# Kernel optimization log

Hardware: AMD Instinct MI355X
Metric: run time of the kernel (lower is better)

The kernel has to match this reference:

```python
import jax, jax.numpy as jnp
import numpy as np
from jax import lax

TOP_K = 6
NORM_MIN = 1e-12


def setup_inputs() -> dict:
    key = jax.random.key(0)
    k0, k1, k2, k3, k4, k5 = jax.random.split(key, 6)
    B, S, H, E, I = 2, 1024, 2048, 64, 512
    return {
        "hidden_states": jax.random.normal(k0, (B, S, H), dtype=jnp.float32),
        "gate_w": jax.random.normal(k1, (E, H), dtype=jnp.float32) * 0.02,
        "e_bias": jax.random.normal(k2, (E,), dtype=jnp.float32) * 0.01,
        "gate_proj": jax.random.normal(k3, (E, H, I), dtype=jnp.float32) * 0.02,
        "up_proj": jax.random.normal(k4, (E, H, I), dtype=jnp.float32) * 0.02,
        "down_proj": jax.random.normal(k5, (E, I, H), dtype=jnp.float32) * 0.02,
    }


def reference(hidden_states, gate_w, e_bias, gate_proj, up_proj, down_proj):
    B, S, H = hidden_states.shape
    E = gate_w.shape[0]
    x = hidden_states.reshape(-1, H)                      # [T, H]
    T = x.shape[0]

    # --- routing (done in float32 in the original) ---
    router_logits = x.astype(jnp.float32) @ gate_w.T      # [T, E]
    routing_probs = jax.nn.softmax(router_logits, axis=-1)
    # topk over bias-corrected scores, but weights come from raw probs
    _, selected = lax.top_k(routing_probs + e_bias[None, :], TOP_K)  # [T, k]
    w = jnp.take_along_axis(routing_probs, selected, axis=-1)        # [T, k]
    w = w / jnp.clip(w.sum(axis=-1, keepdims=True), NORM_MIN)
    w = w.astype(hidden_states.dtype)

    # combine weights: [T, E], zero for unselected experts
    combine = jnp.zeros((T, E), dtype=hidden_states.dtype)
    combine = combine.at[jnp.arange(T)[:, None], selected].add(w)

    # --- experts: SwiGLU MLP per expert, weighted-sum combine ---
    def step(acc, params):
        wg, wu, wd, c = params                            # wg,wu [H,I]; wd [I,H]; c [T]
        h = jax.nn.silu(x @ wg) * (x @ wu)                # [T, I]
        return acc + (h @ wd) * c[:, None], None

    init = jnp.zeros((T, H), dtype=hidden_states.dtype)
    final, _ = lax.scan(step, init, (gate_proj, up_proj, down_proj, combine.T))
    return final.reshape(-1), router_logits.reshape(-1)
```

## Files before the change

### kernel.cpp

```cpp
#include <hip/hip_runtime.h>
#include <math.h>

#define T_TOK 2048
#define H_DIM 2048
#define E_NUM 64
#define I_DIM 512
#define TOPK  6
#define NPAIR (T_TOK * TOPK)
#define MAXTILES 80

typedef __attribute__((ext_vector_type(8))) short s8;
typedef __attribute__((ext_vector_type(4))) float f4;
typedef __attribute__((ext_vector_type(8))) unsigned short u16x8;

static __device__ __forceinline__ unsigned short f2bf(float f) {
  unsigned int u = __float_as_uint(f);
  u += 0x7fff + ((u >> 16) & 1);
  return (unsigned short)(u >> 16);
}
static __device__ __forceinline__ unsigned int cvt_pk(float lo, float hi) {
  unsigned int r;
  asm("v_cvt_pk_bf16_f32 %0, %1, %2" : "=v"(r) : "v"(lo), "v"(hi));
  return r;
}
static __device__ __forceinline__ void gload_lds16(const void* g, void* l) {
  __builtin_amdgcn_global_load_lds(
      (const __attribute__((address_space(1))) unsigned int*)g,
      (__attribute__((address_space(3))) unsigned int*)l, 16, 0, 0);
}
#define SBAR()      __builtin_amdgcn_s_barrier()
#define SCHED0()    __builtin_amdgcn_sched_barrier(0)
#define WAIT_LGKM0() asm volatile("s_waitcnt lgkmcnt(0)" ::: "memory")
#define WAIT_VM0()   asm volatile("s_waitcnt vmcnt(0)" ::: "memory")
#define WAIT_VM2()   asm volatile("s_waitcnt vmcnt(2)" ::: "memory")
#define WAIT_VM4()   asm volatile("s_waitcnt vmcnt(4)" ::: "memory")
#define WAIT_VM6()   asm volatile("s_waitcnt vmcnt(6)" ::: "memory")

__global__ __launch_bounds__(512) void router_kernel(
    const float* __restrict__ x, const float* __restrict__ gw,
    const float* __restrict__ ebias, float* __restrict__ logits_out,
    int* __restrict__ sel, float* __restrict__ wsel)
{
  __shared__ float xs[4][H_DIM];
  __shared__ float lg[4][E_NUM];
  int t0 = blockIdx.x * 4;
  int tid = threadIdx.x;
  {
    float4* xsv = (float4*)&xs[0][0];
    const float4* src = (const float4*)(x + (size_t)t0 * H_DIM);
    for (int i = tid; i < 4 * H_DIM / 4; i += 512) xsv[i] = src[i];
  }
  __syncthreads();

  int wave = tid >> 6, lane = tid & 63;
  for (int ii = 0; ii < 4; ++ii) {
    int e0 = wave * 8 + ii * 2, e1 = e0 + 1;
    const float4* g0 = (const float4*)(gw + (size_t)e0 * H_DIM);
    const float4* g1 = (const float4*)(gw + (size_t)e1 * H_DIM);
    float s00=0.f,s01=0.f,s02=0.f,s03=0.f, s10=0.f,s11=0.f,s12=0.f,s13=0.f;
    for (int h4 = lane; h4 < H_DIM / 4; h4 += 64) {
      float4 w0 = g0[h4], w1 = g1[h4];
      float4 a0 = ((const float4*)xs[0])[h4];
      float4 a1 = ((const float4*)xs[1])[h4];
      float4 a2 = ((const float4*)xs[2])[h4];
      float4 a3 = ((const float4*)xs[3])[h4];
      s00 += w0.x*a0.x + w0.y*a0.y + w0.z*a0.z + w0.w*a0.w;
      s01 += w0.x*a1.x + w0.y*a1.y + w0.z*a1.z + w0.w*a1.w;
      s02 += w0.x*a2.x + w0.y*a2.y + w0.z*a2.z + w0.w*a2.w;
      s03 += w0.x*a3.x + w0.y*a3.y + w0.z*a3.z + w0.w*a3.w;
      s10 += w1.x*a0.x + w1.y*a0.y + w1.z*a0.z + w1.w*a0.w;
      s11 += w1.x*a1.x + w1.y*a1.y + w1.z*a1.z + w1.w*a1.w;
      s12 += w1.x*a2.x + w1.y*a2.y + w1.z*a2.z + w1.w*a2.w;
      s13 += w1.x*a3.x + w1.y*a3.y + w1.z*a3.z + w1.w*a3.w;
    }
    for (int off = 32; off; off >>= 1) {
      s00 += __shfl_down(s00, off); s01 += __shfl_down(s01, off);
      s02 += __shfl_down(s02, off); s03 += __shfl_down(s03, off);
      s10 += __shfl_down(s10, off); s11 += __shfl_down(s11, off);
      s12 += __shfl_down(s12, off); s13 += __shfl_down(s13, off);
    }
    if (lane == 0) {
      lg[0][e0]=s00; lg[1][e0]=s01; lg[2][e0]=s02; lg[3][e0]=s03;
      lg[0][e1]=s10; lg[1][e1]=s11; lg[2][e1]=s12; lg[3][e1]=s13;
    }
  }
  __syncthreads();

  if (tid < 256) {
    int tt = tid >> 6, e = tid & 63;
    logits_out[(size_t)(t0 + tt) * E_NUM + e] = lg[tt][e];
  }

  if (wave == 0) {
    for (int tt = 0; tt < 4; ++tt) {
      int t = t0 + tt;
      float v = lg[tt][lane];
      float m = v;
      for (int off = 32; off; off >>= 1) m = fmaxf(m, __shfl_xor(m, off));
      float ex = __expf(v - m);
      float sum = ex;
      for (int off = 32; off; off >>= 1) sum += __shfl_xor(sum, off);
      float prob = ex / sum;
      float sc = prob + ebias[lane];

      int selidx[TOPK]; float selw[TOPK]; float wsum = 0.f;
      #pragma unroll
      for (int k = 0; k < TOPK; ++k) {
        float mm = sc;
        for (int off = 32; off; off >>= 1) mm = fmaxf(mm, __shfl_xor(mm, off));
        unsigned long long ball = __ballot(sc == mm);
        int s = __ffsll(ball) - 1;
        float p = __shfl(prob, s);
        selidx[k] = s; selw[k] = p; wsum += p;
        if (lane == s) sc = -INFINITY;
      }
      if (lane == 0) {
        float inv = 1.f / fmaxf(wsum, 1e-12f);
        #pragma unroll
        for (int k = 0; k < TOPK; ++k) {
          sel[t * TOPK + k] = selidx[k];
          wsel[t * TOPK + k] = selw[k] * inv;
        }
      }
    }
  }
}

__global__ __launch_bounds__(64) void build_lists(
    const int* __restrict__ sel, const float* __restrict__ wsel,
    int* __restrict__ cnt, int* __restrict__ toklist, float* __restrict__ wtlist,
    int* __restrict__ posmap)
{
  int e = blockIdx.x, lane = threadIdx.x;
  int base = 0;
  for (int t0 = 0; t0 < T_TOK; t0 += 64) {
    int t = t0 + lane;
    int flag = 0, kk = 0; float w = 0.f;
    #pragma unroll
    for (int k = 0; k < TOPK; ++k)
      if (sel[t * TOPK + k] == e) { flag = 1; kk = k; w = wsel[t * TOPK + k]; }
    unsigned long long b = __ballot(flag);
    int pos = base + __popcll(b & ((1ull << lane) - 1ull));
    if (flag) {
      toklist[e * T_TOK + pos] = t;
      wtlist[e * T_TOK + pos] = w;
      posmap[t * TOPK + kk] = pos;
    }
    base += __popcll(b);
  }
  if (lane == 0) cnt[e] = base;
}

__global__ void scan_kernel(const int* __restrict__ cnt, int* __restrict__ texp,
                            int* __restrict__ tmap, int* __restrict__ ntile) {
  if (threadIdx.x == 0) {
    int nt = 0;
    for (int e = 0; e < E_NUM; ++e) {
      texp[e] = nt;
      int m = (cnt[e] + 255) >> 8;
      for (int tb = 0; tb < m && nt < MAXTILES; ++tb) tmap[nt++] = e * 16 + tb;
    }
    *ntile = nt;
  }
}

__global__ __launch_bounds__(256) void permute_kernel(
    const float* __restrict__ x, const int* __restrict__ cnt,
    const int* __restrict__ toklist, const int* __restrict__ tmap,
    const int* __restrict__ ntile, unsigned short* __restrict__ xt)
{
  int tile = blockIdx.y;
  if (tile >= *ntile) return;
  int ks = blockIdx.x;
  int em = tmap[tile], e = em >> 4, tb = em & 15;
  int n = cnt[e];
  int r = threadIdx.x;
  int tok = toklist[e * T_TOK + min(tb * 256 + r, n - 1)];
  const float4* src = (const float4*)(x + (size_t)tok * H_DIM + ks * 32);
  float4 v[8];
  #pragma unroll
  for (int q = 0; q < 8; ++q) v[q] = src[q];
  int g = (r >> 1) & 3;
  unsigned short* dst = xt + ((size_t)(tile * 64 + ks) * 1024 + r * 4) * 8;
  #pragma unroll
  for (int u = 0; u < 4; ++u) {
    int k16 = u ^ g;
    float4 a = v[2 * k16], b = v[2 * k16 + 1];
    u16x8 p;
    ((unsigned int*)&p)[0] = cvt_pk(a.x, a.y);
    ((unsigned int*)&p)[1] = cvt_pk(a.z, a.w);
    ((unsigned int*)&p)[2] = cvt_pk(b.x, b.y);
    ((unsigned int*)&p)[3] = cvt_pk(b.z, b.w);
    *(u16x8*)(dst + u * 8) = p;
  }
}

__global__ __launch_bounds__(512, 4) void gateup_kernel(
    const unsigned short* __restrict__ xt, const float* __restrict__ gp,
    const float* __restrict__ up, const int* __restrict__ tmap,
    const int* __restrict__ ntile, unsigned short* __restrict__ hat)
{
  __shared__ __align__(16) unsigned short A_lds[2][8192];
  __shared__ __align__(16) unsigned int   Bt[2][2][64 * 20];
  int tile = blockIdx.x;
  if (tile >= *ntile) return;
  int e = tmap[tile] >> 4;
  int ic = blockIdx.y, colbase = ic * 64;
  int tid = threadIdx.x, lane = tid & 63, wave = tid >> 6;
  int matc = wave >> 2, cw = wave & 3;
  int lrow = (lane >> 4) * 4, lcol = lane & 15, kgl = lane >> 4;
  int hp = tid & 15, cb = (tid >> 4) & 15, mstage = tid >> 8;
  const float* bsrc0 = ((mstage == 0) ? gp : up)
      + (size_t)e * (H_DIM * I_DIM) + colbase + (size_t)(2 * hp) * I_DIM + cb * 4;
  const unsigned short* achunk0 = xt + (size_t)tile * 64 * 1024 * 8;

  f4 acc[4][4];
  #pragma unroll
  for (int a = 0; a < 4; ++a)
    #pragma unroll
    for (int b = 0; b < 4; ++b) acc[a][b] = (f4)0.f;

  float4 p0, p1, q0, q1;
  {
    const unsigned short* s = achunk0 + (size_t)(wave * 128 + lane) * 8;
    gload_lds16(s,       &A_lds[0][(wave * 128) * 8]);
    gload_lds16(s + 512, &A_lds[0][(wave * 128 + 64) * 8]);
    p0 = *(const float4*)bsrc0;
    p1 = *(const float4*)(bsrc0 + I_DIM);
    WAIT_VM0();
    unsigned int* db = &Bt[0][mstage][cb * 4 * 20 + hp];
    db[0]  = cvt_pk(p0.x, p1.x); db[20] = cvt_pk(p0.y, p1.y);
    db[40] = cvt_pk(p0.z, p1.z); db[60] = cvt_pk(p0.w, p1.w);
    const float* b1 = bsrc0 + (size_t)32 * I_DIM;
    q0 = *(const float4*)b1;
    q1 = *(const float4*)(b1 + I_DIM);
    WAIT_LGKM0();
    SBAR();
    SCHED0();
  }

#define GU_STEP(K, C0, C1, N0, N1) do {                                            \
    if ((K) + 1 < 64) {                                                            \
      const unsigned short* s = achunk0 + ((size_t)((K) + 1) * 1024 + wave * 128 + lane) * 8; \
      gload_lds16(s,       &A_lds[((K) + 1) & 1][(wave * 128) * 8]);               \
      gload_lds16(s + 512, &A_lds[((K) + 1) & 1][(wave * 128 + 64) * 8]);          \
    }                                                                              \
    if ((K) + 2 < 64) {                                                            \
      const float* b = bsrc0 + (size_t)((K) + 2) * 32 * I_DIM;                     \
      N0 = *(const float4*)b; N1 = *(const float4*)(b + I_DIM);                    \
    }                                                                              \
    if ((K) + 2 < 64)      { WAIT_VM4(); }                                         \
    else if ((K) + 1 < 64) { WAIT_VM2(); }                                         \
    else                   { WAIT_VM0(); }                                         \
    if ((K) + 1 < 64) {                                                            \
      unsigned int* db = &Bt[((K) + 1) & 1][mstage][cb * 4 * 20 + hp];             \
      db[0]  = cvt_pk(C0.x, C1.x); db[20] = cvt_pk(C0.y, C1.y);                    \
      db[40] = cvt_pk(C0.z, C1.z); db[60] = cvt_pk(C0.w, C1.w);                    \
    }                                                                              \
    {                                                                              \
      s8 afr[4];                                                                   \
      _Pragma("unroll")                                                            \
      for (int mf = 0; mf < 4; ++mf) {                                             \
        int r = cw * 64 + mf * 16 + lcol;                                          \
        afr[mf] = *(s8*)&A_lds[(K) & 1][r * 32 + ((kgl ^ ((r >> 1) & 3)) * 8)];    \
      }                                                                            \
      _Pragma("unroll")                                                            \
      for (int nf = 0; nf < 4; ++nf) {                                             \
        s8 bfr = *(s8*)&Bt[(K) & 1][matc][(nf * 16 + lcol) * 20 + kgl * 4];        \
        _Pragma("unroll")                                                          \
        for (int mf = 0; mf < 4; ++mf)                                             \
          acc[mf][nf] = __builtin_amdgcn_mfma_f32_16x16x32_bf16(afr[mf], bfr, acc[mf][nf], 0, 0, 0); \
      }                                                                            \
    }                                                                              \
    if ((K) + 1 < 64) {                                                            \
      if ((K) + 2 < 64) { WAIT_VM2(); } else { WAIT_VM0(); }                       \
      WAIT_LGKM0(); SBAR(); SCHED0();                                              \
    }                                                                              \
  } while (0)

  for (int k = 0; k < 64; k += 2) {
    GU_STEP(k,     q0, q1, p0, p1);
    GU_STEP(k + 1, p0, p1, q0, q1);
  }
#undef GU_STEP

  f4* exch = (f4*)&Bt[0][0][0];
  unsigned short* hs = &A_lds[0][0];
  #pragma unroll
  for (int nf = 0; nf < 4; ++nf) {
    __syncthreads();
    if (wave >= 4) {
      #pragma unroll
      for (int mf = 0; mf < 4; ++mf)
        exch[((wave - 4) * 4 + mf) * 64 + lane] = acc[mf][nf];
    }
    __syncthreads();
    if (wave < 4) {
      #pragma unroll
      for (int mf = 0; mf < 4; ++mf) {
        f4 u = exch[(wave * 4 + mf) * 64 + lane];
        #pragma unroll
        for (int j = 0; j < 4; ++j) {
          float g = acc[mf][nf][j];
          float h = g / (1.f + __expf(-g)) * u[j];
          hs[(wave * 64 + mf * 16 + lrow + j) * 64 + nf * 16 + lcol] = f2bf(h);
        }
      }
    }
  }
  __syncthreads();
  #pragma unroll
  for (int c = 0; c < 2; ++c) {
    unsigned short* base = hat + (size_t)(tile * 16 + ic * 2 + c) * 1024 * 8;
    for (int uu = tid; uu < 1024; uu += 512) {
      int row = uu >> 2, k16 = (uu & 3) ^ ((row >> 1) & 3);
      *(u16x8*)(base + (size_t)uu * 8) = *(const u16x8*)&hs[row * 64 + c * 32 + k16 * 8];
    }
  }
}

__global__ __launch_bounds__(256, 4) void down_kernel(
    const unsigned short* __restrict__ hat, const float* __restrict__ dp,
    const int* __restrict__ cnt, const int* __restrict__ tmap,
    const int* __restrict__ ntile, const float* __restrict__ wtlist,
    unsigned short* __restrict__ pout)
{
  __shared__ __align__(16) unsigned short A_lds[2][8192];
  __shared__ __align__(16) unsigned int   Bt[2][64 * 20];
  __shared__ float swt[256];
  int tile = blockIdx.x;
  if (tile >= *ntile) return;
  int em = tmap[tile], e = em >> 4, tb = em & 15;
  int n = cnt[e];
  int hc = blockIdx.y, colbase = hc * 64;
  int tid = threadIdx.x, lane = tid & 63, wave = tid >> 6, wbase = wave * 64;
  int lrow = (lane >> 4) * 4, lcol = lane & 15, kgl = lane >> 4;
  int hp = tid & 15, cb = tid >> 4;
  const float* bsrc0 = dp + (size_t)e * (I_DIM * H_DIM) + colbase
                       + (size_t)(2 * hp) * H_DIM + cb * 4;
  const unsigned short* achunk0 = hat + (size_t)tile * 16 * 1024 * 8;

  int rr = tb * 256 + tid;
  swt[tid] = (rr < n) ? wtlist[e * T_TOK + rr] : 0.f;

  f4 acc[4][4];
  #pragma unroll
  for (int a = 0; a < 4; ++a)
    #pragma unroll
    for (int b = 0; b < 4; ++b) acc[a][b] = (f4)0.f;

  float4 p0, p1, q0, q1;
  {
    const unsigned short* s = achunk0 + (size_t)(wave * 256 + lane) * 8;
    #pragma unroll
    for (int i = 0; i < 4; ++i)
      gload_lds16(s + i * 512, &A_lds[0][(wave * 256 + i * 64) * 8]);
    p0 = *(const float4*)bsrc0;
    p1 = *(const float4*)(bsrc0 + H_DIM);
    WAIT_VM0();
    unsigned int* db = &Bt[0][cb * 4 * 20 + hp];
    db[0]  = cvt_pk(p0.x, p1.x); db[20] = cvt_pk(p0.y, p1.y);
    db[40] = cvt_pk(p0.z, p1.z); db[60] = cvt_pk(p0.w, p1.w);
    const float* b1 = bsrc0 + (size_t)32 * H_DIM;
    q0 = *(const float4*)b1;
    q1 = *(const float4*)(b1 + H_DIM);
    WAIT_LGKM0();
    SBAR();
    SCHED0();
  }

#define DN_STEP(K, C0, C1, N0, N1) do {                                            \
    if ((K) + 1 < 16) {                                                            \
      const unsigned short* s = achunk0 + ((size_t)((K) + 1) * 1024 + wave * 256 + lane) * 8; \
      _Pragma("unroll")                                                            \
      for (int i = 0; i < 4; ++i)                                                  \
        gload_lds16(s + i * 512, &A_lds[((K) + 1) & 1][(wave * 256 + i * 64) * 8]);\
    }                                                                              \
    if ((K) + 2 < 16) {                                                            \
      const float* b = bsrc0 + (size_t)((K) + 2) * 32 * H_DIM;                     \
      N0 = *(const float4*)b; N1 = *(const float4*)(b + H_DIM);                    \
    }                                                                              \
    if ((K) + 2 < 16)      { WAIT_VM6(); }                                         \
    else if ((K) + 1 < 16) { WAIT_VM4(); }                                         \
    else                   { WAIT_VM0(); }                                         \
    if ((K) + 1 < 16) {                                                            \
      unsigned int* db = &Bt[((K) + 1) & 1][cb * 4 * 20 + hp];                     \
      db[0]  = cvt_pk(C0.x, C1.x); db[20] = cvt_pk(C0.y, C1.y);                    \
      db[40] = cvt_pk(C0.z, C1.z); db[60] = cvt_pk(C0.w, C1.w);                    \
    }                                                                              \
    {                                                                              \
      s8 afr[4];                                                                   \
      _Pragma("unroll")                                                            \
      for (int mf = 0; mf < 4; ++mf) {                                             \
        int r = wbase + mf * 16 + lcol;                                            \
        afr[mf] = *(s8*)&A_lds[(K) & 1][r * 32 + ((kgl ^ ((r >> 1) & 3)) * 8)];    \
      }                                                                            \
      _Pragma("unroll")                                                            \
      for (int nf = 0; nf < 4; ++nf) {                                             \
        s8 bfr = *(s8*)&Bt[(K) & 1][(nf * 16 + lcol) * 20 + kgl * 4];              \
        _Pragma("unroll")                                                          \
        for (int mf = 0; mf < 4; ++mf)                                             \
          acc[mf][nf] = __builtin_amdgcn_mfma_f32_16x16x32_bf16(afr[mf], bfr, acc[mf][nf], 0, 0, 0); \
      }                                                                            \
    }                                                                              \
    if ((K) + 1 < 16) {                                                            \
      if ((K) + 2 < 16) { WAIT_VM2(); } else { WAIT_VM0(); }                       \
      WAIT_LGKM0(); SBAR(); SCHED0();                                              \
    }                                                                              \
  } while (0)

  for (int k = 0; k < 16; k += 2) {
    DN_STEP(k,     q0, q1, p0, p1);
    DN_STEP(k + 1, p0, p1, q0, q1);
  }
#undef DN_STEP

  __syncthreads();
  unsigned short* hs = &A_lds[0][0];
  #pragma unroll
  for (int mf = 0; mf < 4; ++mf)
    #pragma unroll
    for (int nf = 0; nf < 4; ++nf)
      #pragma unroll
      for (int j = 0; j < 4; ++j) {
        int r = wbase + mf * 16 + lrow + j;
        hs[r * 64 + nf * 16 + lcol] = f2bf(acc[mf][nf][j] * swt[r]);
      }
  __syncthreads();
  for (int u = tid; u < 2048; u += 256) {
    int row = u >> 3, unit = u & 7;
    *(u16x8*)(pout + (size_t)(tile * 256 + row) * H_DIM + colbase + unit * 8) =
        *(const u16x8*)&hs[row * 64 + unit * 8];
  }
}

__global__ __launch_bounds__(256) void reduce_kernel(
    const unsigned short* __restrict__ pout, const int* __restrict__ sel,
    const int* __restrict__ posmap, const int* __restrict__ texp,
    float* __restrict__ out)
{
  int t = blockIdx.x, tid = threadIdx.x;
  int col = tid * 8;
  float acc[8];
  #pragma unroll
  for (int j = 0; j < 8; ++j) acc[j] = 0.f;
  #pragma unroll
  for (int k = 0; k < TOPK; ++k) {
    int e = sel[t * TOPK + k];
    int row = texp[e] * 256 + posmap[t * TOPK + k];
    u16x8 v = *(const u16x8*)(pout + (size_t)row * H_DIM + col);
    #pragma unroll
    for (int j = 0; j < 8; ++j)
      acc[j] += __uint_as_float((unsigned int)(unsigned short)v[j] << 16);
  }
  float4 o0 = {acc[0], acc[1], acc[2], acc[3]};
  float4 o1 = {acc[4], acc[5], acc[6], acc[7]};
  *(float4*)(out + (size_t)t * H_DIM + col)     = o0;
  *(float4*)(out + (size_t)t * H_DIM + col + 4) = o1;
}

extern "C" void kernel_launch(void* const* d_in, const int* in_sizes, int n_in,
                              void* d_out, int out_size, void* d_ws, size_t ws_size,
                              hipStream_t stream) {
  const float* hidden = (const float*)d_in[0];
  const float* gate_w = (const float*)d_in[1];
  const float* e_bias = (const float*)d_in[2];
  const float* gate_p = (const float*)d_in[3];
  const float* up_p   = (const float*)d_in[4];
  const float* down_p = (const float*)d_in[5];

  float* out_final  = (float*)d_out;
  float* out_logits = out_final + (size_t)T_TOK * H_DIM;

  int*   cnt     = (int*)d_ws;
  int*   texp    = cnt + 64;
  int*   ntile   = texp + 64;
  int*   tmap    = ntile + 16;
  int*   sel     = tmap + MAXTILES;
  float* wsel    = (float*)(sel + NPAIR);
  int*   posmap  = (int*)(wsel + NPAIR);
  int*   toklist = posmap + NPAIR;
  float* wtlist  = (float*)(toklist + E_NUM * T_TOK);
  unsigned short* xt  = (unsigned short*)(wtlist + E_NUM * T_TOK);
  unsigned short* hat = xt + (size_t)MAXTILES * 64 * 1024 * 8;
  unsigned short* pout = xt;

  router_kernel<<<T_TOK / 4, 512, 0, stream>>>(hidden, gate_w, e_bias, out_logits, sel, wsel);
  build_lists<<<E_NUM, 64, 0, stream>>>(sel, wsel, cnt, toklist, wtlist, posmap);
  scan_kernel<<<1, 64, 0, stream>>>(cnt, texp, tmap, ntile);
  permute_kernel<<<dim3(64, MAXTILES), 256, 0, stream>>>(hidden, cnt, toklist, tmap, ntile, xt);
  gateup_kernel<<<dim3(MAXTILES, I_DIM / 64), 512, 0, stream>>>(
      xt, gate_p, up_p, tmap, ntile, hat);
  down_kernel<<<dim3(MAXTILES, H_DIM / 64), 256, 0, stream>>>(
      hat, down_p, cnt, tmap, ntile, wtlist, pout);
  reduce_kernel<<<T_TOK, 256, 0, stream>>>(pout, sel, posmap, texp, out_final);
}
```

Before: 536.2 us.

## Widen down_kernel tile to 128 columns with 512 threads sharing A tile

The down-projection kernel now uses 512 threads per block covering 128 output columns, split into two column groups of four waves that share one staged A (activation) tile in LDS. Each A chunk is loaded once per block instead of once per 64 columns, which halves the A-traffic and the number of blocks. The epilogue writes the two column halves in two passes through the reused LDS buffer, adding barriers. Launch bounds of 512 threads with 4 blocks per SM may raise register pressure and lower occupancy.

```diff
diff --git a/kernel.cpp b/kernel.cpp
--- a/kernel.cpp
+++ b/kernel.cpp
@@ -34,7 +34,6 @@
 #define WAIT_VM0()   asm volatile("s_waitcnt vmcnt(0)" ::: "memory")
 #define WAIT_VM2()   asm volatile("s_waitcnt vmcnt(2)" ::: "memory")
 #define WAIT_VM4()   asm volatile("s_waitcnt vmcnt(4)" ::: "memory")
-#define WAIT_VM6()   asm volatile("s_waitcnt vmcnt(6)" ::: "memory")
 
 __global__ __launch_bounds__(512) void router_kernel(
     const float* __restrict__ x, const float* __restrict__ gw,
@@ -319,29 +318,32 @@
   }
 }
 
-__global__ __launch_bounds__(256, 4) void down_kernel(
+__global__ __launch_bounds__(512, 4) void down_kernel(
     const unsigned short* __restrict__ hat, const float* __restrict__ dp,
     const int* __restrict__ cnt, const int* __restrict__ tmap,
     const int* __restrict__ ntile, const float* __restrict__ wtlist,
     unsigned short* __restrict__ pout)
 {
   __shared__ __align__(16) unsigned short A_lds[2][8192];
-  __shared__ __align__(16) unsigned int   Bt[2][64 * 20];
+  __shared__ __align__(16) unsigned int   Bt[2][2][64 * 20];
   __shared__ float swt[256];
   int tile = blockIdx.x;
   if (tile >= *ntile) return;
   int em = tmap[tile], e = em >> 4, tb = em & 15;
   int n = cnt[e];
-  int hc = blockIdx.y, colbase = hc * 64;
-  int tid = threadIdx.x, lane = tid & 63, wave = tid >> 6, wbase = wave * 64;
+  int hc = blockIdx.y, colbase = hc * 128;
+  int tid = threadIdx.x, lane = tid & 63, wave = tid >> 6;
+  int rg = wave & 3, cg = wave >> 2;
   int lrow = (lane >> 4) * 4, lcol = lane & 15, kgl = lane >> 4;
-  int hp = tid & 15, cb = tid >> 4;
-  const float* bsrc0 = dp + (size_t)e * (I_DIM * H_DIM) + colbase
+  int hp = tid & 15, cb = (tid >> 4) & 15, cgs = tid >> 8;
+  const float* bsrc0 = dp + (size_t)e * (I_DIM * H_DIM) + colbase + cgs * 64
                        + (size_t)(2 * hp) * H_DIM + cb * 4;
   const unsigned short* achunk0 = hat + (size_t)tile * 16 * 1024 * 8;
 
-  int rr = tb * 256 + tid;
-  swt[tid] = (rr < n) ? wtlist[e * T_TOK + rr] : 0.f;
+  if (tid < 256) {
+    int rr = tb * 256 + tid;
+    swt[tid] = (rr < n) ? wtlist[e * T_TOK + rr] : 0.f;
+  }
 
   f4 acc[4][4];
   #pragma unroll
@@ -351,14 +353,13 @@
 
   float4 p0, p1, q0, q1;
   {
-    const unsigned short* s = achunk0 + (size_t)(wave * 256 + lane) * 8;
-    #pragma unroll
-    for (int i = 0; i < 4; ++i)
-      gload_lds16(s + i * 512, &A_lds[0][(wave * 256 + i * 64) * 8]);
+    const unsigned short* s = achunk0 + (size_t)(wave * 128 + lane) * 8;
+    gload_lds16(s,       &A_lds[0][(wave * 128) * 8]);
+    gload_lds16(s + 512, &A_lds[0][(wave * 128 + 64) * 8]);
     p0 = *(const float4*)bsrc0;
     p1 = *(const float4*)(bsrc0 + H_DIM);
     WAIT_VM0();
-    unsigned int* db = &Bt[0][cb * 4 * 20 + hp];
+    unsigned int* db = &Bt[0][cgs][cb * 4 * 20 + hp];
     db[0]  = cvt_pk(p0.x, p1.x); db[20] = cvt_pk(p0.y, p1.y);
     db[40] = cvt_pk(p0.z, p1.z); db[60] = cvt_pk(p0.w, p1.w);
     const float* b1 = bsrc0 + (size_t)32 * H_DIM;
@@ -371,20 +372,19 @@
 
 #define DN_STEP(K, C0, C1, N0, N1) do {                                            \
     if ((K) + 1 < 16) {                                                            \
-      const unsigned short* s = achunk0 + ((size_t)((K) + 1) * 1024 + wave * 256 + lane) * 8; \
-      _Pragma("unroll")                                                            \
-      for (int i = 0; i < 4; ++i)                                                  \
-        gload_lds16(s + i * 512, &A_lds[((K) + 1) & 1][(wave * 256 + i * 64) * 8]);\
+      const unsigned short* s = achunk0 + ((size_t)((K) + 1) * 1024 + wave * 128 + lane) * 8; \
+      gload_lds16(s,       &A_lds[((K) + 1) & 1][(wave * 128) * 8]);               \
+      gload_lds16(s + 512, &A_lds[((K) + 1) & 1][(wave * 128 + 64) * 8]);          \
     }                                                                              \
     if ((K) + 2 < 16) {                                                            \
       const float* b = bsrc0 + (size_t)((K) + 2) * 32 * H_DIM;                     \
       N0 = *(const float4*)b; N1 = *(const float4*)(b + H_DIM);                    \
     }                                                                              \
-    if ((K) + 2 < 16)      { WAIT_VM6(); }                                         \
-    else if ((K) + 1 < 16) { WAIT_VM4(); }                                         \
+    if ((K) + 2 < 16)      { WAIT_VM4(); }                                         \
+    else if ((K) + 1 < 16) { WAIT_VM2(); }                                         \
     else                   { WAIT_VM0(); }                                         \
     if ((K) + 1 < 16) {                                                            \
-      unsigned int* db = &Bt[((K) + 1) & 1][cb * 4 * 20 + hp];                     \
+      unsigned int* db = &Bt[((K) + 1) & 1][cgs][cb * 4 * 20 + hp];                \
       db[0]  = cvt_pk(C0.x, C1.x); db[20] = cvt_pk(C0.y, C1.y);                    \
       db[40] = cvt_pk(C0.z, C1.z); db[60] = cvt_pk(C0.w, C1.w);                    \
     }                                                                              \
@@ -392,12 +392,12 @@
       s8 afr[4];                                                                   \
       _Pragma("unroll")                                                            \
       for (int mf = 0; mf < 4; ++mf) {                                             \
-        int r = wbase + mf * 16 + lcol;                                            \
+        int r = rg * 64 + mf * 16 + lcol;                                          \
         afr[mf] = *(s8*)&A_lds[(K) & 1][r * 32 + ((kgl ^ ((r >> 1) & 3)) * 8)];    \
       }                                                                            \
       _Pragma("unroll")                                                            \
       for (int nf = 0; nf < 4; ++nf) {                                             \
-        s8 bfr = *(s8*)&Bt[(K) & 1][(nf * 16 + lcol) * 20 + kgl * 4];              \
+        s8 bfr = *(s8*)&Bt[(K) & 1][cg][(nf * 16 + lcol) * 20 + kgl * 4];          \
         _Pragma("unroll")                                                          \
         for (int mf = 0; mf < 4; ++mf)                                             \
           acc[mf][nf] = __builtin_amdgcn_mfma_f32_16x16x32_bf16(afr[mf], bfr, acc[mf][nf], 0, 0, 0); \
@@ -418,19 +418,25 @@
   __syncthreads();
   unsigned short* hs = &A_lds[0][0];
   #pragma unroll
-  for (int mf = 0; mf < 4; ++mf)
-    #pragma unroll
-    for (int nf = 0; nf < 4; ++nf)
+  for (int pass = 0; pass < 2; ++pass) {
+    if (cg == pass) {
       #pragma unroll
-      for (int j = 0; j < 4; ++j) {
-        int r = wbase + mf * 16 + lrow + j;
-        hs[r * 64 + nf * 16 + lcol] = f2bf(acc[mf][nf][j] * swt[r]);
-      }
-  __syncthreads();
-  for (int u = tid; u < 2048; u += 256) {
-    int row = u >> 3, unit = u & 7;
-    *(u16x8*)(pout + (size_t)(tile * 256 + row) * H_DIM + colbase + unit * 8) =
-        *(const u16x8*)&hs[row * 64 + unit * 8];
+      for (int mf = 0; mf < 4; ++mf)
+        #pragma unroll
+        for (int nf = 0; nf < 4; ++nf)
+          #pragma unroll
+          for (int j = 0; j < 4; ++j) {
+            int r = rg * 64 + mf * 16 + lrow + j;
+            hs[r * 64 + nf * 16 + lcol] = f2bf(acc[mf][nf][j] * swt[r]);
+          }
+    }
+    __syncthreads();
+    for (int u = tid; u < 2048; u += 512) {
+      int row = u >> 3, unit = u & 7;
+      *(u16x8*)(pout + (size_t)(tile * 256 + row) * H_DIM + colbase + pass * 64 + unit * 8) =
+          *(const u16x8*)&hs[row * 64 + unit * 8];
+    }
+    __syncthreads();
   }
 }
 
@@ -491,7 +497,7 @@
   permute_kernel<<<dim3(64, MAXTILES), 256, 0, stream>>>(hidden, cnt, toklist, tmap, ntile, xt);
   gateup_kernel<<<dim3(MAXTILES, I_DIM / 64), 512, 0, stream>>>(
       xt, gate_p, up_p, tmap, ntile, hat);
-  down_kernel<<<dim3(MAXTILES, H_DIM / 64), 256, 0, stream>>>(
+  down_kernel<<<dim3(MAXTILES, H_DIM / 128), 512, 0, stream>>>(
       hat, down_p, cnt, tmap, ntile, wtlist, pout);
   reduce_kernel<<<T_TOK, 256, 0, stream>>>(pout, sel, posmap, texp, out_final);
 }
```

After: 520.3 us. 1.03x faster.

## Split gate/up GEMM into separate blocks and add standalone SwiGLU kernel

Applied to the files above, without the earlier changes.

The fused 512-thread gate+up kernel, where each block computed both matrices and exchanged accumulators through LDS, becomes a 256-thread kernel that computes one matrix per block, with the matrix chosen by a new grid z dimension. Gate and up outputs go to a bf16 scratch buffer, and a new swiglu kernel combines them into the swizzled layout the down kernel expects. This doubles the number of blocks and removes the multi-barrier exchange epilogue, which could improve occupancy and scheduling. In exchange it adds a kernel launch and an extra global round trip for the intermediates. The intermediates are also rounded to bf16 before the SiLU, which changes numerics slightly. The down kernel also swaps its cb/hp thread index mapping.

```diff
diff --git a/kernel.cpp b/kernel.cpp
--- a/kernel.cpp
+++ b/kernel.cpp
@@ -17,6 +17,9 @@
   unsigned int u = __float_as_uint(f);
   u += 0x7fff + ((u >> 16) & 1);
   return (unsigned short)(u >> 16);
+}
+static __device__ __forceinline__ float bf2f(unsigned short v) {
+  return __uint_as_float((unsigned int)v << 16);
 }
 static __device__ __forceinline__ unsigned int cvt_pk(float lo, float hi) {
   unsigned int r;
@@ -195,22 +198,22 @@
   }
 }
 
-__global__ __launch_bounds__(512, 4) void gateup_kernel(
+__global__ __launch_bounds__(256, 4) void gu_kernel(
     const unsigned short* __restrict__ xt, const float* __restrict__ gp,
     const float* __restrict__ up, const int* __restrict__ tmap,
-    const int* __restrict__ ntile, unsigned short* __restrict__ hat)
+    const int* __restrict__ ntile, unsigned short* __restrict__ gub)
 {
   __shared__ __align__(16) unsigned short A_lds[2][8192];
-  __shared__ __align__(16) unsigned int   Bt[2][2][64 * 20];
+  __shared__ __align__(16) unsigned int   Bt[2][64 * 20];
   int tile = blockIdx.x;
   if (tile >= *ntile) return;
   int e = tmap[tile] >> 4;
-  int ic = blockIdx.y, colbase = ic * 64;
+  int ic = blockIdx.y, mat = blockIdx.z, colbase = ic * 64;
   int tid = threadIdx.x, lane = tid & 63, wave = tid >> 6;
-  int matc = wave >> 2, cw = wave & 3;
+  int cw = wave;
   int lrow = (lane >> 4) * 4, lcol = lane & 15, kgl = lane >> 4;
-  int hp = tid & 15, cb = (tid >> 4) & 15, mstage = tid >> 8;
-  const float* bsrc0 = ((mstage == 0) ? gp : up)
+  int cb = tid & 15, hp = tid >> 4;
+  const float* bsrc0 = (mat ? up : gp)
       + (size_t)e * (H_DIM * I_DIM) + colbase + (size_t)(2 * hp) * I_DIM + cb * 4;
   const unsigned short* achunk0 = xt + (size_t)tile * 64 * 1024 * 8;
 
@@ -222,13 +225,14 @@
 
   float4 p0, p1, q0, q1;
   {
-    const unsigned short* s = achunk0 + (size_t)(wave * 128 + lane) * 8;
-    gload_lds16(s,       &A_lds[0][(wave * 128) * 8]);
-    gload_lds16(s + 512, &A_lds[0][(wave * 128 + 64) * 8]);
+    const unsigned short* s = achunk0 + (size_t)(wave * 256 + lane) * 8;
+    #pragma unroll
+    for (int i = 0; i < 4; ++i)
+      gload_lds16(s + i * 512, &A_lds[0][(wave * 256 + i * 64) * 8]);
     p0 = *(const float4*)bsrc0;
     p1 = *(const float4*)(bsrc0 + I_DIM);
     WAIT_VM0();
-    unsigned int* db = &Bt[0][mstage][cb * 4 * 20 + hp];
+    unsigned int* db = &Bt[0][cb * 4 * 20 + hp];
     db[0]  = cvt_pk(p0.x, p1.x); db[20] = cvt_pk(p0.y, p1.y);
     db[40] = cvt_pk(p0.z, p1.z); db[60] = cvt_pk(p0.w, p1.w);
     const float* b1 = bsrc0 + (size_t)32 * I_DIM;
@@ -241,19 +245,20 @@
 
 #define GU_STEP(K, C0, C1, N0, N1) do {                                            \
     if ((K) + 1 < 64) {                                                            \
-      const unsigned short* s = achunk0 + ((size_t)((K) + 1) * 1024 + wave * 128 + lane) * 8; \
-      gload_lds16(s,       &A_lds[((K) + 1) & 1][(wave * 128) * 8]);               \
-      gload_lds16(s + 512, &A_lds[((K) + 1) & 1][(wave * 128 + 64) * 8]);          \
+      const unsigned short* s = achunk0 + ((size_t)((K) + 1) * 1024 + wave * 256 + lane) * 8; \
+      _Pragma("unroll")                                                            \
+      for (int i = 0; i < 4; ++i)                                                  \
+        gload_lds16(s + i * 512, &A_lds[((K) + 1) & 1][(wave * 256 + i * 64) * 8]);\
     }                                                                              \
     if ((K) + 2 < 64) {                                                            \
       const float* b = bsrc0 + (size_t)((K) + 2) * 32 * I_DIM;                     \
       N0 = *(const float4*)b; N1 = *(const float4*)(b + I_DIM);                    \
     }                                                                              \
-    if ((K) + 2 < 64)      { WAIT_VM4(); }                                         \
-    else if ((K) + 1 < 64) { WAIT_VM2(); }                                         \
+    if ((K) + 2 < 64)      { WAIT_VM6(); }                                         \
+    else if ((K) + 1 < 64) { WAIT_VM4(); }                                         \
     else                   { WAIT_VM0(); }                                         \
     if ((K) + 1 < 64) {                                                            \
-      unsigned int* db = &Bt[((K) + 1) & 1][mstage][cb * 4 * 20 + hp];             \
+      unsigned int* db = &Bt[((K) + 1) & 1][cb * 4 * 20 + hp];                     \
       db[0]  = cvt_pk(C0.x, C1.x); db[20] = cvt_pk(C0.y, C1.y);                    \
       db[40] = cvt_pk(C0.z, C1.z); db[60] = cvt_pk(C0.w, C1.w);                    \
     }                                                                              \
@@ -266,7 +271,7 @@
       }                                                                            \
       _Pragma("unroll")                                                            \
       for (int nf = 0; nf < 4; ++nf) {                                             \
-        s8 bfr = *(s8*)&Bt[(K) & 1][matc][(nf * 16 + lcol) * 20 + kgl * 4];        \
+        s8 bfr = *(s8*)&Bt[(K) & 1][(nf * 16 + lcol) * 20 + kgl * 4];              \
         _Pragma("unroll")                                                          \
         for (int mf = 0; mf < 4; ++mf)                                             \
           acc[mf][nf] = __builtin_amdgcn_mfma_f32_16x16x32_bf16(afr[mf], bfr, acc[mf][nf], 0, 0, 0); \
@@ -284,38 +289,49 @@
   }
 #undef GU_STEP
 
-  f4* exch = (f4*)&Bt[0][0][0];
+  __syncthreads();
   unsigned short* hs = &A_lds[0][0];
   #pragma unroll
-  for (int nf = 0; nf < 4; ++nf) {
-    __syncthreads();
-    if (wave >= 4) {
+  for (int mf = 0; mf < 4; ++mf)
+    #pragma unroll
+    for (int nf = 0; nf < 4; ++nf)
       #pragma unroll
-      for (int mf = 0; mf < 4; ++mf)
-        exch[((wave - 4) * 4 + mf) * 64 + lane] = acc[mf][nf];
-    }
-    __syncthreads();
-    if (wave < 4) {
-      #pragma unroll
-      for (int mf = 0; mf < 4; ++mf) {
-        f4 u = exch[(wave * 4 + mf) * 64 + lane];
-        #pragma unroll
-        for (int j = 0; j < 4; ++j) {
-          float g = acc[mf][nf][j];
-          float h = g / (1.f + __expf(-g)) * u[j];
-          hs[(wave * 64 + mf * 16 + lrow + j) * 64 + nf * 16 + lcol] = f2bf(h);
-        }
+      for (int j = 0; j < 4; ++j) {
+        int r = cw * 64 + mf * 16 + lrow + j;
+        hs[r * 64 + nf * 16 + lcol] = f2bf(acc[mf][nf][j]);
       }
-    }
-  }
   __syncthreads();
-  #pragma unroll
-  for (int c = 0; c < 2; ++c) {
-    unsigned short* base = hat + (size_t)(tile * 16 + ic * 2 + c) * 1024 * 8;
-    for (int uu = tid; uu < 1024; uu += 512) {
-      int row = uu >> 2, k16 = (uu & 3) ^ ((row >> 1) & 3);
-      *(u16x8*)(base + (size_t)uu * 8) = *(const u16x8*)&hs[row * 64 + c * 32 + k16 * 8];
-    }
+  unsigned short* base = gub + ((size_t)((mat * MAXTILES + tile) * 8 + ic)) * 16384;
+  for (int u = tid; u < 2048; u += 256) {
+    int row = u >> 3, unit = u & 7;
+    *(u16x8*)(base + (size_t)row * 64 + unit * 8) = *(const u16x8*)&hs[row * 64 + unit * 8];
+  }
+}
+
+__global__ __launch_bounds__(256) void swiglu_kernel(
+    const unsigned short* __restrict__ gub, const int* __restrict__ ntile,
+    unsigned short* __restrict__ hat)
+{
+  int tile = blockIdx.y;
+  if (tile >= *ntile) return;
+  int c = blockIdx.x;
+  int ic = c >> 1, half = c & 1;
+  const unsigned short* gsrc = gub + ((size_t)(tile * 8 + ic)) * 16384;
+  const unsigned short* usrc = gsrc + (size_t)MAXTILES * 8 * 16384;
+  unsigned short* dst = hat + (size_t)(tile * 16 + c) * 1024 * 8;
+  for (int uu = threadIdx.x; uu < 1024; uu += 256) {
+    int row = uu >> 2, k16 = (uu & 3) ^ ((row >> 1) & 3);
+    size_t off = (size_t)row * 64 + half * 32 + k16 * 8;
+    u16x8 gv = *(const u16x8*)(gsrc + off);
+    u16x8 uv = *(const u16x8*)(usrc + off);
+    u16x8 hv;
+    #pragma unroll
+    for (int j = 0; j < 8; ++j) {
+      float gf = bf2f((unsigned short)gv[j]);
+      float uf = bf2f((unsigned short)uv[j]);
+      hv[j] = f2bf(gf / (1.f + __expf(-gf)) * uf);
+    }
+    *(u16x8*)(dst + (size_t)uu * 8) = hv;
   }
 }
 
@@ -333,9 +349,10 @@
   int em = tmap[tile], e = em >> 4, tb = em & 15;
   int n = cnt[e];
   int hc = blockIdx.y, colbase = hc * 64;
-  int tid = threadIdx.x, lane = tid & 63, wave = tid >> 6, wbase = wave * 64;
+  int tid = threadIdx.x, lane = tid & 63, wave = tid >> 6;
+  int wbase = wave * 64;
   int lrow = (lane >> 4) * 4, lcol = lane & 15, kgl = lane >> 4;
-  int hp = tid & 15, cb = tid >> 4;
+  int cb = tid & 15, hp = tid >> 4;
   const float* bsrc0 = dp + (size_t)e * (I_DIM * H_DIM) + colbase
                        + (size_t)(2 * hp) * H_DIM + cb * 4;
   const unsigned short* achunk0 = hat + (size_t)tile * 16 * 1024 * 8;
@@ -483,14 +500,16 @@
   float* wtlist  = (float*)(toklist + E_NUM * T_TOK);
   unsigned short* xt  = (unsigned short*)(wtlist + E_NUM * T_TOK);
   unsigned short* hat = xt + (size_t)MAXTILES * 64 * 1024 * 8;
+  unsigned short* gub = hat + (size_t)MAXTILES * 16 * 1024 * 8;
   unsigned short* pout = xt;
 
   router_kernel<<<T_TOK / 4, 512, 0, stream>>>(hidden, gate_w, e_bias, out_logits, sel, wsel);
   build_lists<<<E_NUM, 64, 0, stream>>>(sel, wsel, cnt, toklist, wtlist, posmap);
   scan_kernel<<<1, 64, 0, stream>>>(cnt, texp, tmap, ntile);
   permute_kernel<<<dim3(64, MAXTILES), 256, 0, stream>>>(hidden, cnt, toklist, tmap, ntile, xt);
-  gateup_kernel<<<dim3(MAXTILES, I_DIM / 64), 512, 0, stream>>>(
-      xt, gate_p, up_p, tmap, ntile, hat);
+  gu_kernel<<<dim3(MAXTILES, I_DIM / 64, 2), 256, 0, stream>>>(
+      xt, gate_p, up_p, tmap, ntile, gub);
+  swiglu_kernel<<<dim3(16, MAXTILES), 256, 0, stream>>>(gub, ntile, hat);
   down_kernel<<<dim3(MAXTILES, H_DIM / 64), 256, 0, stream>>>(
       hat, down_p, cnt, tmap, ntile, wtlist, pout);
   reduce_kernel<<<T_TOK, 256, 0, stream>>>(pout, sel, posmap, texp, out_final);
```

New measurement: 547.9 us. 2.2% more time.
